# Kernel tuning notes

Measured on AMD Instinct MI355X. Metric: run time of the kernel, lower is better.

The kernel has to match this reference:

```python
import jax, jax.numpy as jnp
import numpy as np

NEG_SLOPE = 0.01  # torch F.leaky_relu default


def _graph_conv(x, W, b, src, dst, n_dst):
    """DGL GraphConv, norm='both': out = D_dst^{-1/2} A^T (D_src^{-1/2} x W) + b.
    Degrees clamped to min 1 (DGL behavior). src/dst are edge endpoint indices.
    """
    n_src = x.shape[0]
    ones = jnp.ones(src.shape[0], dtype=x.dtype)
    out_deg = jnp.zeros(n_src, dtype=x.dtype).at[src].add(ones)
    in_deg = jnp.zeros(n_dst, dtype=x.dtype).at[dst].add(ones)
    inv_s = jax.lax.rsqrt(jnp.maximum(out_deg, 1.0))
    inv_d = jax.lax.rsqrt(jnp.maximum(in_deg, 1.0))
    # weight first (in_feats >= out_feats path in DGL; math identical either way)
    feat = (x * inv_s[:, None]) @ W                      # [n_src, out]
    agg = jax.ops.segment_sum(feat[src], dst, num_segments=n_dst)  # SpMM
    return agg * inv_d[:, None] + b


def setup_inputs() -> dict:
    key = jax.random.key(0)
    ks = jax.random.split(key, 16)
    Nc, Ng, F, H, O = 50000, 30000, 128, 128, 128
    Ecc, Ecg, Egc = 500000, 400000, 400000
    inp = {
        "x_chem": jax.random.normal(ks[0], (Nc, F), jnp.float32),
        "x_gene": jax.random.normal(ks[1], (Ng, F), jnp.float32),
        "src_cc": jax.random.randint(ks[2], (Ecc,), 0, Nc, jnp.int32),
        "dst_cc": jax.random.randint(ks[3], (Ecc,), 0, Nc, jnp.int32),
        "src_cg": jax.random.randint(ks[4], (Ecg,), 0, Nc, jnp.int32),
        "dst_cg": jax.random.randint(ks[5], (Ecg,), 0, Ng, jnp.int32),
        "src_gc": jax.random.randint(ks[6], (Egc,), 0, Ng, jnp.int32),
        "dst_gc": jax.random.randint(ks[7], (Egc,), 0, Nc, jnp.int32),
    }
    scale1 = 1.0 / np.sqrt(F)
    scale2 = 1.0 / np.sqrt(H)
    inp["W1_cc"] = jax.random.normal(ks[8], (F, H), jnp.float32) * scale1
    inp["W1_cg"] = jax.random.normal(ks[9], (F, H), jnp.float32) * scale1
    inp["W1_gc"] = jax.random.normal(ks[10], (F, H), jnp.float32) * scale1
    inp["W2_cc"] = jax.random.normal(ks[11], (H, O), jnp.float32) * scale2
    inp["W2_cg"] = jax.random.normal(ks[12], (H, O), jnp.float32) * scale2
    inp["W2_gc"] = jax.random.normal(ks[13], (H, O), jnp.float32) * scale2
    for name, d in [("b1_cc", H), ("b1_cg", H), ("b1_gc", H), ("b2_cc", O), ("b2_cg", O), ("b2_gc", O)]:
        inp[name] = jnp.zeros((d,), jnp.float32)
    return inp


def reference(x_chem, x_gene, src_cc, dst_cc, src_cg, dst_cg, src_gc, dst_gc,
              W1_cc, b1_cc, W1_cg, b1_cg, W1_gc, b1_gc,
              W2_cc, b2_cc, W2_cg, b2_cg, W2_gc, b2_gc):
    Nc, Ng = x_chem.shape[0], x_gene.shape[0]
    # --- layer 1: HeteroGraphConv with sum aggregation across relations ---
    h1_chem = (_graph_conv(x_chem, W1_cc, b1_cc, src_cc, dst_cc, Nc)
               + _graph_conv(x_gene, W1_gc, b1_gc, src_gc, dst_gc, Nc))
    h1_gene = _graph_conv(x_chem, W1_cg, b1_cg, src_cg, dst_cg, Ng)
    h1_chem = jax.nn.leaky_relu(h1_chem, NEG_SLOPE)
    h1_gene = jax.nn.leaky_relu(h1_gene, NEG_SLOPE)
    # --- layer 2 ---
    h2_chem = (_graph_conv(h1_chem, W2_cc, b2_cc, src_cc, dst_cc, Nc)
               + _graph_conv(h1_gene, W2_gc, b2_gc, src_gc, dst_gc, Nc))
    return h2_chem
```

## Files before the change

kernel.cpp:

```cpp
#include <hip/hip_runtime.h>
#include <math.h>

#define NEG_SLOPE 0.01f
#define ELLW 40

typedef float f4 __attribute__((ext_vector_type(4)));
typedef __bf16 bf16x8 __attribute__((ext_vector_type(8)));
typedef __bf16 bf16x4 __attribute__((ext_vector_type(4)));
typedef _Float16 h4 __attribute__((ext_vector_type(4)));
typedef _Float16 h8 __attribute__((ext_vector_type(8)));

__global__ __launch_bounds__(256) void prep_w_zero(
    const float* __restrict__ W0, const float* __restrict__ W1,
    const float* __restrict__ W2, const float* __restrict__ W3,
    const float* __restrict__ W4, __bf16* __restrict__ H, __bf16* __restrict__ L,
    int* __restrict__ zp, int zN)
{
    const int b = blockIdx.x;
    if (b < 320) {
        const int y = b >> 6;
        const float* W = y == 0 ? W0 : y == 1 ? W1 : y == 2 ? W2 : y == 3 ? W3 : W4;
        int idx = (b & 63) * 256 + threadIdx.x;
        int k = idx >> 7, n = idx & 127;
        float w = W[idx];
        __bf16 h = (__bf16)w;
        __bf16 l = (__bf16)(w - (float)h);
        H[(size_t)y * 16384 + n * 128 + k] = h;
        L[(size_t)y * 16384 + n * 128 + k] = l;
    } else {
        int i = (b - 320) * 256 + threadIdx.x;
        if (i < zN) zp[i] = 0;
    }
}

template <int RELU, typename T>
__device__ __forceinline__ void gemm_core(const T* __restrict__ A,
    const __bf16* __restrict__ Bh, const __bf16* __restrict__ Bl,
    _Float16* __restrict__ C, int M, int row0, int tid,
    __bf16 (*Ah)[136], __bf16 (*Al)[136])
{
    if constexpr (sizeof(T) == 4) {
#pragma unroll
        for (int it = 0; it < 8; ++it) {
            int idx4 = it * 256 + tid;
            int r = idx4 >> 5;
            int c = (idx4 & 31) << 2;
            int rg = row0 + r;
            f4 v = {0.f, 0.f, 0.f, 0.f};
            if (rg < M) v = *(const f4*)(A + (size_t)rg * 128 + c);
            if (RELU) {
#pragma unroll
                for (int j = 0; j < 4; ++j) v[j] = v[j] >= 0.f ? v[j] : v[j] * NEG_SLOPE;
            }
            bf16x4 hv, lv;
#pragma unroll
            for (int j = 0; j < 4; ++j) {
                __bf16 h = (__bf16)v[j];
                hv[j] = h;
                lv[j] = (__bf16)(v[j] - (float)h);
            }
            *(bf16x4*)&Ah[r][c] = hv;
            *(bf16x4*)&Al[r][c] = lv;
        }
    } else {
#pragma unroll
        for (int it = 0; it < 4; ++it) {
            int idx8 = it * 256 + tid;
            int r = idx8 >> 4;
            int c = (idx8 & 15) << 3;
            int rg = row0 + r;
            h8 v8 = {};
            if (rg < M) v8 = *(const h8*)(A + (size_t)rg * 128 + c);
            bf16x8 hv, lv;
#pragma unroll
            for (int j = 0; j < 8; ++j) {
                float v = (float)v8[j];
                if (RELU) v = v >= 0.f ? v : v * NEG_SLOPE;
                __bf16 h = (__bf16)v;
                hv[j] = h;
                lv[j] = (__bf16)(v - (float)h);
            }
            *(bf16x8*)&Ah[r][c] = hv;
            *(bf16x8*)&Al[r][c] = lv;
        }
    }
    __syncthreads();

    const int lane = tid & 63;
    const int wid = tid >> 6;
    const int lm = lane & 15;
    const int lq = lane >> 4;
    const int mbase = (wid & 1) * 32;
    const int nbase = (wid >> 1) * 64;

    f4 acc[2][4] = {};
#pragma unroll
    for (int kc = 0; kc < 4; ++kc) {
        const int koff = kc * 32 + lq * 8;
        bf16x8 ah[2], al[2], bh[4], bl[4];
#pragma unroll
        for (int mi = 0; mi < 2; ++mi) {
            ah[mi] = *(const bf16x8*)&Ah[mbase + mi * 16 + lm][koff];
            al[mi] = *(const bf16x8*)&Al[mbase + mi * 16 + lm][koff];
        }
#pragma unroll
        for (int ni = 0; ni < 4; ++ni) {
            size_t boff = (size_t)(nbase + ni * 16 + lm) * 128 + koff;
            bh[ni] = *(const bf16x8*)(Bh + boff);
            bl[ni] = *(const bf16x8*)(Bl + boff);
        }
#pragma unroll
        for (int mi = 0; mi < 2; ++mi)
#pragma unroll
            for (int ni = 0; ni < 4; ++ni) {
                acc[mi][ni] = __builtin_amdgcn_mfma_f32_16x16x32_bf16(ah[mi], bh[ni], acc[mi][ni], 0, 0, 0);
                acc[mi][ni] = __builtin_amdgcn_mfma_f32_16x16x32_bf16(al[mi], bh[ni], acc[mi][ni], 0, 0, 0);
                acc[mi][ni] = __builtin_amdgcn_mfma_f32_16x16x32_bf16(ah[mi], bl[ni], acc[mi][ni], 0, 0, 0);
            }
    }

#pragma unroll
    for (int mi = 0; mi < 2; ++mi) {
        int rbase = row0 + mbase + mi * 16 + lq * 4;
#pragma unroll
        for (int r = 0; r < 4; ++r) {
            int row = rbase + r;
            if (row < M) {
#pragma unroll
                for (int ni = 0; ni < 4; ++ni)
                    C[(size_t)row * 128 + nbase + ni * 16 + lm] = (_Float16)acc[mi][ni][r];
            }
        }
    }
}

__global__ __launch_bounds__(256) void fused_build_gemm(
    const int* __restrict__ s0, const int* __restrict__ d0, int* sd0, int* c0, unsigned short* e0, int E0, int B0,
    const int* __restrict__ s1, const int* __restrict__ d1, int* sd1, int* c1, unsigned short* e1, int E1, int B1,
    const int* __restrict__ s2, const int* __restrict__ d2, int* sd2, int* c2, unsigned short* e2, int E2,
    const float* __restrict__ xc, const float* __restrict__ xg,
    const __bf16* __restrict__ wt_h, const __bf16* __restrict__ wt_l,
    _Float16* __restrict__ t_cg, _Float16* __restrict__ t_cc, _Float16* __restrict__ t_gc,
    int Nc, int Ng, int gBc, int G, int EB)
{
    __shared__ __bf16 Ah[64][136];
    __shared__ __bf16 Al[64][136];
    const int idx = blockIdx.x;
    const int r7 = idx % 7, q = idx / 7;
    if (r7 < 2) {
        int g = q * 2 + r7;
        if (g >= G) return;
        if (g < gBc)
            gemm_core<0>(xc, wt_h, wt_l, t_cg, Nc, g * 64, threadIdx.x, Ah, Al);
        else if (g < 2 * gBc)
            gemm_core<0>(xc, wt_h + 16384, wt_l + 16384, t_cc, Nc, (g - gBc) * 64, threadIdx.x, Ah, Al);
        else
            gemm_core<0>(xg, wt_h + 2 * 16384, wt_l + 2 * 16384, t_gc, Ng, (g - 2 * gBc) * 64, threadIdx.x, Ah, Al);
    } else {
        int eb = q * 5 + (r7 - 2);
        if (eb >= EB) return;
        const int* src; const int* dst; int* sdeg; int* cnt; unsigned short* ell; int E; int base;
        if (eb < B0)            { src = s0; dst = d0; sdeg = sd0; cnt = c0; ell = e0; E = E0; base = eb; }
        else if (eb < B0 + B1)  { src = s1; dst = d1; sdeg = sd1; cnt = c1; ell = e1; E = E1; base = eb - B0; }
        else                    { src = s2; dst = d2; sdeg = sd2; cnt = c2; ell = e2; E = E2; base = eb - B0 - B1; }
        int i0 = base * 512 + threadIdx.x;
        int i1 = i0 + 256;
        int sa = -1, da = 0, sb = -1, db = 0;
        if (i0 < E) { sa = src[i0]; da = dst[i0]; }
        if (i1 < E) { sb = src[i1]; db = dst[i1]; }
        if (sa >= 0) atomicAdd(&sdeg[sa], 1);
        if (sb >= 0) atomicAdd(&sdeg[sb], 1);
        if (sa >= 0) {
            int p = atomicAdd(&cnt[da], 1);
            if (p < ELLW) ell[da * ELLW + p] = (unsigned short)sa;
        }
        if (sb >= 0) {
            int p = atomicAdd(&cnt[db], 1);
            if (p < ELLW) ell[db * ELLW + p] = (unsigned short)sb;
        }
    }
}

__global__ __launch_bounds__(256) void gemm2_both(
    const _Float16* __restrict__ h1c, const _Float16* __restrict__ h1g,
    const __bf16* __restrict__ wt_h, const __bf16* __restrict__ wt_l,
    _Float16* __restrict__ t_cc, _Float16* __restrict__ t_gc, int Nc, int Ng, int gBc)
{
    __shared__ __bf16 Ah[64][136];
    __shared__ __bf16 Al[64][136];
    if ((int)blockIdx.x < gBc)
        gemm_core<1>(h1c, wt_h + 3 * 16384, wt_l + 3 * 16384, t_cc, Nc, blockIdx.x * 64, threadIdx.x, Ah, Al);
    else
        gemm_core<1>(h1g, wt_h + 4 * 16384, wt_l + 4 * 16384, t_gc, Ng, (blockIdx.x - gBc) * 64, threadIdx.x, Ah, Al);
}

__device__ __forceinline__ void rel_accum8(const _Float16* __restrict__ feat,
    const unsigned short* __restrict__ cp, int n, const int* __restrict__ sdeg,
    int grp, int c8, float* acc)
{
    int i = grp;
    for (; i + 4 < n; i += 8) {
        int q0 = cp[i], q1 = cp[i + 4];
        float w0 = rsqrtf(fmaxf((float)sdeg[q0], 1.0f));
        float w1 = rsqrtf(fmaxf((float)sdeg[q1], 1.0f));
        h8 v0 = *(const h8*)(feat + (size_t)q0 * 128 + c8);
        h8 v1 = *(const h8*)(feat + (size_t)q1 * 128 + c8);
#pragma unroll
        for (int j = 0; j < 8; ++j) acc[j] += (float)v0[j] * w0;
#pragma unroll
        for (int j = 0; j < 8; ++j) acc[j] += (float)v1[j] * w1;
    }
    if (i < n) {
        int q0 = cp[i];
        float w0 = rsqrtf(fmaxf((float)sdeg[q0], 1.0f));
        h8 v0 = *(const h8*)(feat + (size_t)q0 * 128 + c8);
#pragma unroll
        for (int j = 0; j < 8; ++j) acc[j] += (float)v0[j] * w0;
    }
}

__device__ __forceinline__ void xgrp_sum8(float* a)
{
#pragma unroll
    for (int j = 0; j < 8; ++j) {
        a[j] += __shfl_xor(a[j], 16);
        a[j] += __shfl_xor(a[j], 32);
    }
}

__global__ __launch_bounds__(256) void gather_l1(
    const _Float16* __restrict__ t_cg, const unsigned short* __restrict__ ell_cg,
    const int* __restrict__ cnt_cg, const int* __restrict__ degs_cg,
    const _Float16* __restrict__ f_cc, const unsigned short* __restrict__ ell_cc,
    const int* __restrict__ cnt_cc, const int* __restrict__ degs_cc,
    const _Float16* __restrict__ t_gc, const unsigned short* __restrict__ ell_gc,
    const int* __restrict__ cnt_gc, const int* __restrict__ degs_gc,
    const float* __restrict__ b1_cg, const float* __restrict__ b1_cc, const float* __restrict__ b1_gc,
    _Float16* __restrict__ h1_gene, _Float16* __restrict__ h1_chem, int Ng, int Nc, int Bg)
{
    const int lane = threadIdx.x & 63;
    const int grp = lane >> 4;
    const int c8 = (lane & 15) << 3;
    if ((int)blockIdx.x < Bg) {
        int row = blockIdx.x * 4 + (threadIdx.x >> 6);
        if (row >= Ng) return;
        int n = cnt_cg[row];
        float wd = rsqrtf(fmaxf((float)n, 1.0f));
        if (n > ELLW) n = ELLW;
        float acc[8] = {};
        rel_accum8(t_cg, ell_cg + row * ELLW, n, degs_cg, grp, c8, acc);
#pragma unroll
        for (int j = 0; j < 8; ++j) acc[j] *= wd;
        xgrp_sum8(acc);
        if (grp == 0) {
            f4 blo = *(const f4*)(b1_cg + c8);
            f4 bhi = *(const f4*)(b1_cg + c8 + 4);
            h8 o;
#pragma unroll
            for (int j = 0; j < 4; ++j) o[j] = (_Float16)(acc[j] + blo[j]);
#pragma unroll
            for (int j = 0; j < 4; ++j) o[4 + j] = (_Float16)(acc[4 + j] + bhi[j]);
            *(h8*)(h1_gene + (size_t)row * 128 + c8) = o;
        }
    } else {
        int row = (blockIdx.x - Bg) * 4 + (threadIdx.x >> 6);
        if (row >= Nc) return;
        int na = cnt_cc[row];
        float wa = rsqrtf(fmaxf((float)na, 1.0f));
        if (na > ELLW) na = ELLW;
        float accA[8] = {};
        rel_accum8(f_cc, ell_cc + row * ELLW, na, degs_cc, grp, c8, accA);
        int nb = cnt_gc[row];
        float wb = rsqrtf(fmaxf((float)nb, 1.0f));
        if (nb > ELLW) nb = ELLW;
        float accB[8] = {};
        rel_accum8(t_gc, ell_gc + row * ELLW, nb, degs_gc, grp, c8, accB);
        float r[8];
#pragma unroll
        for (int j = 0; j < 8; ++j) r[j] = accA[j] * wa + accB[j] * wb;
        xgrp_sum8(r);
        if (grp == 0) {
            f4 b0lo = *(const f4*)(b1_cc + c8);
            f4 b0hi = *(const f4*)(b1_cc + c8 + 4);
            f4 b1lo = *(const f4*)(b1_gc + c8);
            f4 b1hi = *(const f4*)(b1_gc + c8 + 4);
            h8 o;
#pragma unroll
            for (int j = 0; j < 4; ++j) o[j] = (_Float16)(r[j] + b0lo[j] + b1lo[j]);
#pragma unroll
            for (int j = 0; j < 4; ++j) o[4 + j] = (_Float16)(r[4 + j] + b0hi[j] + b1hi[j]);
            *(h8*)(h1_chem + (size_t)row * 128 + c8) = o;
        }
    }
}

__global__ __launch_bounds__(256) void gather_l2(
    const _Float16* __restrict__ fA, const unsigned short* __restrict__ ellA,
    const int* __restrict__ cntA, const int* __restrict__ degsA,
    const _Float16* __restrict__ fB, const unsigned short* __restrict__ ellB,
    const int* __restrict__ cntB, const int* __restrict__ degsB,
    const float* __restrict__ bA, const float* __restrict__ bB,
    float* __restrict__ out, int Nd)
{
    const int lane = threadIdx.x & 63;
    const int grp = lane >> 4;
    const int c8 = (lane & 15) << 3;
    int row = blockIdx.x * 4 + (threadIdx.x >> 6);
    if (row >= Nd) return;
    int na = cntA[row];
    float wa = rsqrtf(fmaxf((float)na, 1.0f));
    if (na > ELLW) na = ELLW;
    float accA[8] = {};
    rel_accum8(fA, ellA + row * ELLW, na, degsA, grp, c8, accA);
    int nb = cntB[row];
    float wb = rsqrtf(fmaxf((float)nb, 1.0f));
    if (nb > ELLW) nb = ELLW;
    float accB[8] = {};
    rel_accum8(fB, ellB + row * ELLW, nb, degsB, grp, c8, accB);
    float r[8];
#pragma unroll
    for (int j = 0; j < 8; ++j) r[j] = accA[j] * wa + accB[j] * wb;
    xgrp_sum8(r);
    if (grp == 0) {
        f4 balo = *(const f4*)(bA + c8);
        f4 bahi = *(const f4*)(bA + c8 + 4);
        f4 bblo = *(const f4*)(bB + c8);
        f4 bbhi = *(const f4*)(bB + c8 + 4);
        f4 olo, ohi;
#pragma unroll
        for (int j = 0; j < 4; ++j) olo[j] = r[j] + balo[j] + bblo[j];
#pragma unroll
        for (int j = 0; j < 4; ++j) ohi[j] = r[4 + j] + bahi[j] + bbhi[j];
        *(f4*)(out + (size_t)row * 128 + c8) = olo;
        *(f4*)(out + (size_t)row * 128 + c8 + 4) = ohi;
    }
}

extern "C" void kernel_launch(void* const* d_in, const int* in_sizes, int n_in,
                              void* d_out, int out_size, void* d_ws, size_t ws_size,
                              hipStream_t stream)
{
    const float* x_chem = (const float*)d_in[0];
    const float* x_gene = (const float*)d_in[1];
    const int* src_cc = (const int*)d_in[2];
    const int* dst_cc = (const int*)d_in[3];
    const int* src_cg = (const int*)d_in[4];
    const int* dst_cg = (const int*)d_in[5];
    const int* src_gc = (const int*)d_in[6];
    const int* dst_gc = (const int*)d_in[7];
    const float* W1_cc = (const float*)d_in[8];
    const float* W1_cg = (const float*)d_in[9];
    const float* W1_gc = (const float*)d_in[10];
    const float* W2_cc = (const float*)d_in[11];
    const float* W2_gc = (const float*)d_in[13];
    const float* b1_cc = (const float*)d_in[14];
    const float* b1_cg = (const float*)d_in[15];
    const float* b1_gc = (const float*)d_in[16];
    const float* b2_cc = (const float*)d_in[17];
    const float* b2_gc = (const float*)d_in[19];
    (void)n_in; (void)out_size; (void)ws_size;

    const int Nc = in_sizes[0] / 128;
    const int Ng = in_sizes[1] / 128;
    const int Ecc = in_sizes[2];
    const int Ecg = in_sizes[4];
    const int Egc = in_sizes[6];

    int* cnt_cc  = (int*)d_ws;
    int* cnt_cg  = cnt_cc + Nc;
    int* cnt_gc  = cnt_cg + Ng;
    int* degs_cc = cnt_gc + Nc;
    int* degs_cg = degs_cc + Nc;
    int* degs_gc = degs_cg + Nc;
    const int degTotal = 4 * Nc + 2 * Ng;
    unsigned short* ell_cc = (unsigned short*)(degs_gc + Ng);
    unsigned short* ell_cg = ell_cc + (size_t)Nc * ELLW;
    unsigned short* ell_gc = ell_cg + (size_t)Ng * ELLW;
    size_t off = (size_t)((char*)(ell_gc + (size_t)Nc * ELLW) - (char*)d_ws);
    off = (off + 255) & ~(size_t)255;
    _Float16* h1_chem = (_Float16*)((char*)d_ws + off);
    _Float16* h1_gene = h1_chem + (size_t)Nc * 128;
    _Float16* tmp_cg  = h1_gene + (size_t)Ng * 128;
    _Float16* tmp_gc  = tmp_cg + (size_t)Nc * 128;
    _Float16* tmp_cc  = tmp_gc + (size_t)Ng * 128;
    __bf16* wt_h = (__bf16*)(tmp_cc + (size_t)Nc * 128);
    __bf16* wt_l = wt_h + 5 * 16384;
    float* outF = (float*)d_out;

    dim3 blk(256);
    const int B0 = (Ecc + 511) / 512, B1 = (Ecg + 511) / 512, B2 = (Egc + 511) / 512;
    const int EB = B0 + B1 + B2;
    const int gBc = (Nc + 63) / 64, gBg = (Ng + 63) / 64;
    const int G = 2 * gBc + gBg;
    int Q = (G + 1) / 2;
    if ((EB + 4) / 5 > Q) Q = (EB + 4) / 5;
    const int T = 7 * Q;

    const int zB = (degTotal + 255) / 256;
    prep_w_zero<<<320 + zB, blk, 0, stream>>>(W1_cg, W1_cc, W1_gc, W2_cc, W2_gc,
        wt_h, wt_l, (int*)d_ws, degTotal);

    fused_build_gemm<<<T, blk, 0, stream>>>(
        src_cc, dst_cc, degs_cc, cnt_cc, ell_cc, Ecc, B0,
        src_cg, dst_cg, degs_cg, cnt_cg, ell_cg, Ecg, B1,
        src_gc, dst_gc, degs_gc, cnt_gc, ell_gc, Egc,
        x_chem, x_gene, wt_h, wt_l, tmp_cg, tmp_cc, tmp_gc,
        Nc, Ng, gBc, G, EB);

    const int Bg = (Ng + 3) / 4, Bc = (Nc + 3) / 4;
    gather_l1<<<Bg + Bc, blk, 0, stream>>>(
        tmp_cg, ell_cg, cnt_cg, degs_cg,
        tmp_cc, ell_cc, cnt_cc, degs_cc,
        tmp_gc, ell_gc, cnt_gc, degs_gc,
        b1_cg, b1_cc, b1_gc, h1_gene, h1_chem, Ng, Nc, Bg);

    gemm2_both<<<gBc + gBg, blk, 0, stream>>>(h1_chem, h1_gene, wt_h, wt_l,
        tmp_cg, tmp_gc, Nc, Ng, gBc);

    gather_l2<<<Bc, blk, 0, stream>>>(
        tmp_cg, ell_cc, cnt_cc, degs_cc,
        tmp_gc, ell_gc, cnt_gc, degs_gc,
        b2_cc, b2_gc, outF, Nc);
}
```

Measured before the change: 373.9 us.

## Pre-scale feature tables by source-degree norm instead of per-edge rsqrt in gathers

Moves the D_src^{-1/2} normalisation out of the per-edge gather loops. Layer-1 tables are rescaled in a new scale_tables pass, and layer-2 tables get the factor in the GEMM epilogue. The gathers then drop the per-edge random sdeg loads and rsqrt, at the cost of an extra read-modify-write pass over the layer-1 tables and one extra launch. The edge-build blocks also drop from 512 to 256 edges per block, which doubles their count.

```diff
diff --git a/kernel.cpp b/kernel.cpp
--- a/kernel.cpp
+++ b/kernel.cpp
@@ -33,10 +33,10 @@
     }
 }
 
-template <int RELU, typename T>
+template <int RELU, int SCALE, typename T>
 __device__ __forceinline__ void gemm_core(const T* __restrict__ A,
     const __bf16* __restrict__ Bh, const __bf16* __restrict__ Bl,
-    _Float16* __restrict__ C, int M, int row0, int tid,
+    _Float16* __restrict__ C, const int* __restrict__ rdeg, int M, int row0, int tid,
     __bf16 (*Ah)[136], __bf16 (*Al)[136])
 {
     if constexpr (sizeof(T) == 4) {
@@ -126,9 +126,11 @@
         for (int r = 0; r < 4; ++r) {
             int row = rbase + r;
             if (row < M) {
+                float s = 1.0f;
+                if (SCALE) s = rsqrtf(fmaxf((float)rdeg[row], 1.0f));
 #pragma unroll
                 for (int ni = 0; ni < 4; ++ni)
-                    C[(size_t)row * 128 + nbase + ni * 16 + lm] = (_Float16)acc[mi][ni][r];
+                    C[(size_t)row * 128 + nbase + ni * 16 + lm] = (_Float16)(acc[mi][ni][r] * s);
             }
         }
     }
@@ -151,11 +153,11 @@
         int g = q * 2 + r7;
         if (g >= G) return;
         if (g < gBc)
-            gemm_core<0>(xc, wt_h, wt_l, t_cg, Nc, g * 64, threadIdx.x, Ah, Al);
+            gemm_core<0, 0>(xc, wt_h, wt_l, t_cg, (const int*)nullptr, Nc, g * 64, threadIdx.x, Ah, Al);
         else if (g < 2 * gBc)
-            gemm_core<0>(xc, wt_h + 16384, wt_l + 16384, t_cc, Nc, (g - gBc) * 64, threadIdx.x, Ah, Al);
+            gemm_core<0, 0>(xc, wt_h + 16384, wt_l + 16384, t_cc, (const int*)nullptr, Nc, (g - gBc) * 64, threadIdx.x, Ah, Al);
         else
-            gemm_core<0>(xg, wt_h + 2 * 16384, wt_l + 2 * 16384, t_gc, Ng, (g - 2 * gBc) * 64, threadIdx.x, Ah, Al);
+            gemm_core<0, 0>(xg, wt_h + 2 * 16384, wt_l + 2 * 16384, t_gc, (const int*)nullptr, Ng, (g - 2 * gBc) * 64, threadIdx.x, Ah, Al);
     } else {
         int eb = q * 5 + (r7 - 2);
         if (eb >= EB) return;
@@ -163,59 +165,73 @@
         if (eb < B0)            { src = s0; dst = d0; sdeg = sd0; cnt = c0; ell = e0; E = E0; base = eb; }
         else if (eb < B0 + B1)  { src = s1; dst = d1; sdeg = sd1; cnt = c1; ell = e1; E = E1; base = eb - B0; }
         else                    { src = s2; dst = d2; sdeg = sd2; cnt = c2; ell = e2; E = E2; base = eb - B0 - B1; }
-        int i0 = base * 512 + threadIdx.x;
-        int i1 = i0 + 256;
-        int sa = -1, da = 0, sb = -1, db = 0;
-        if (i0 < E) { sa = src[i0]; da = dst[i0]; }
-        if (i1 < E) { sb = src[i1]; db = dst[i1]; }
-        if (sa >= 0) atomicAdd(&sdeg[sa], 1);
-        if (sb >= 0) atomicAdd(&sdeg[sb], 1);
-        if (sa >= 0) {
-            int p = atomicAdd(&cnt[da], 1);
-            if (p < ELLW) ell[da * ELLW + p] = (unsigned short)sa;
-        }
-        if (sb >= 0) {
-            int p = atomicAdd(&cnt[db], 1);
-            if (p < ELLW) ell[db * ELLW + p] = (unsigned short)sb;
-        }
-    }
+        int i = base * 256 + threadIdx.x;
+        if (i < E) {
+            int s = src[i];
+            int d = dst[i];
+            atomicAdd(&sdeg[s], 1);
+            int p = atomicAdd(&cnt[d], 1);
+            if (p < ELLW) ell[d * ELLW + p] = (unsigned short)s;
+        }
+    }
+}
+
+__global__ __launch_bounds__(256) void scale_tables(
+    _Float16* __restrict__ t_cg, const int* __restrict__ degs_cg,
+    _Float16* __restrict__ t_cc, const int* __restrict__ degs_cc,
+    _Float16* __restrict__ t_gc, const int* __restrict__ degs_gc,
+    int Nc, int Ng)
+{
+    int idx = blockIdx.x * 256 + threadIdx.x;
+    int gr = idx >> 4;
+    int c8 = (idx & 15) << 3;
+    int total = 2 * Nc + Ng;
+    if (gr >= total) return;
+    _Float16* p;
+    int deg;
+    if (gr < Nc)            { p = t_cg + (size_t)gr * 128 + c8;            deg = degs_cg[gr]; }
+    else if (gr < 2 * Nc)   { p = t_cc + (size_t)(gr - Nc) * 128 + c8;     deg = degs_cc[gr - Nc]; }
+    else                    { p = t_gc + (size_t)(gr - 2 * Nc) * 128 + c8; deg = degs_gc[gr - 2 * Nc]; }
+    float s = rsqrtf(fmaxf((float)deg, 1.0f));
+    h8 v = *(const h8*)p;
+#pragma unroll
+    for (int j = 0; j < 8; ++j) v[j] = (_Float16)((float)v[j] * s);
+    *(h8*)p = v;
 }
 
 __global__ __launch_bounds__(256) void gemm2_both(
     const _Float16* __restrict__ h1c, const _Float16* __restrict__ h1g,
     const __bf16* __restrict__ wt_h, const __bf16* __restrict__ wt_l,
+    const int* __restrict__ degs_cc, const int* __restrict__ degs_gc,
     _Float16* __restrict__ t_cc, _Float16* __restrict__ t_gc, int Nc, int Ng, int gBc)
 {
     __shared__ __bf16 Ah[64][136];
     __shared__ __bf16 Al[64][136];
     if ((int)blockIdx.x < gBc)
-        gemm_core<1>(h1c, wt_h + 3 * 16384, wt_l + 3 * 16384, t_cc, Nc, blockIdx.x * 64, threadIdx.x, Ah, Al);
+        gemm_core<1, 1>(h1c, wt_h + 3 * 16384, wt_l + 3 * 16384, t_cc, degs_cc, Nc, blockIdx.x * 64, threadIdx.x, Ah, Al);
     else
-        gemm_core<1>(h1g, wt_h + 4 * 16384, wt_l + 4 * 16384, t_gc, Ng, (blockIdx.x - gBc) * 64, threadIdx.x, Ah, Al);
+        gemm_core<1, 1>(h1g, wt_h + 4 * 16384, wt_l + 4 * 16384, t_gc, degs_gc, Ng, (blockIdx.x - gBc) * 64, threadIdx.x, Ah, Al);
 }
 
 __device__ __forceinline__ void rel_accum8(const _Float16* __restrict__ feat,
-    const unsigned short* __restrict__ cp, int n, const int* __restrict__ sdeg,
+    const unsigned short* __restrict__ cp, int n,
     int grp, int c8, float* acc)
 {
     int i = grp;
     for (; i + 4 < n; i += 8) {
         int q0 = cp[i], q1 = cp[i + 4];
-        float w0 = rsqrtf(fmaxf((float)sdeg[q0], 1.0f));
-        float w1 = rsqrtf(fmaxf((float)sdeg[q1], 1.0f));
         h8 v0 = *(const h8*)(feat + (size_t)q0 * 128 + c8);
         h8 v1 = *(const h8*)(feat + (size_t)q1 * 128 + c8);
 #pragma unroll
-        for (int j = 0; j < 8; ++j) acc[j] += (float)v0[j] * w0;
-#pragma unroll
-        for (int j = 0; j < 8; ++j) acc[j] += (float)v1[j] * w1;
+        for (int j = 0; j < 8; ++j) acc[j] += (float)v0[j];
+#pragma unroll
+        for (int j = 0; j < 8; ++j) acc[j] += (float)v1[j];
     }
     if (i < n) {
         int q0 = cp[i];
-        float w0 = rsqrtf(fmaxf((float)sdeg[q0], 1.0f));
         h8 v0 = *(const h8*)(feat + (size_t)q0 * 128 + c8);
 #pragma unroll
-        for (int j = 0; j < 8; ++j) acc[j] += (float)v0[j] * w0;
+        for (int j = 0; j < 8; ++j) acc[j] += (float)v0[j];
     }
 }
 
@@ -230,11 +246,11 @@
 
 __global__ __launch_bounds__(256) void gather_l1(
     const _Float16* __restrict__ t_cg, const unsigned short* __restrict__ ell_cg,
-    const int* __restrict__ cnt_cg, const int* __restrict__ degs_cg,
+    const int* __restrict__ cnt_cg,
     const _Float16* __restrict__ f_cc, const unsigned short* __restrict__ ell_cc,
-    const int* __restrict__ cnt_cc, const int* __restrict__ degs_cc,
+    const int* __restrict__ cnt_cc,
     const _Float16* __restrict__ t_gc, const unsigned short* __restrict__ ell_gc,
-    const int* __restrict__ cnt_gc, const int* __restrict__ degs_gc,
+    const int* __restrict__ cnt_gc,
     const float* __restrict__ b1_cg, const float* __restrict__ b1_cc, const float* __restrict__ b1_gc,
     _Float16* __restrict__ h1_gene, _Float16* __restrict__ h1_chem, int Ng, int Nc, int Bg)
 {
@@ -248,7 +264,7 @@
         float wd = rsqrtf(fmaxf((float)n, 1.0f));
         if (n > ELLW) n = ELLW;
         float acc[8] = {};
-        rel_accum8(t_cg, ell_cg + row * ELLW, n, degs_cg, grp, c8, acc);
+        rel_accum8(t_cg, ell_cg + row * ELLW, n, grp, c8, acc);
 #pragma unroll
         for (int j = 0; j < 8; ++j) acc[j] *= wd;
         xgrp_sum8(acc);
@@ -269,12 +285,12 @@
         float wa = rsqrtf(fmaxf((float)na, 1.0f));
         if (na > ELLW) na = ELLW;
         float accA[8] = {};
-        rel_accum8(f_cc, ell_cc + row * ELLW, na, degs_cc, grp, c8, accA);
+        rel_accum8(f_cc, ell_cc + row * ELLW, na, grp, c8, accA);
         int nb = cnt_gc[row];
         float wb = rsqrtf(fmaxf((float)nb, 1.0f));
         if (nb > ELLW) nb = ELLW;
         float accB[8] = {};
-        rel_accum8(t_gc, ell_gc + row * ELLW, nb, degs_gc, grp, c8, accB);
+        rel_accum8(t_gc, ell_gc + row * ELLW, nb, grp, c8, accB);
         float r[8];
 #pragma unroll
         for (int j = 0; j < 8; ++j) r[j] = accA[j] * wa + accB[j] * wb;
@@ -296,9 +312,9 @@
 
 __global__ __launch_bounds__(256) void gather_l2(
     const _Float16* __restrict__ fA, const unsigned short* __restrict__ ellA,
-    const int* __restrict__ cntA, const int* __restrict__ degsA,
+    const int* __restrict__ cntA,
     const _Float16* __restrict__ fB, const unsigned short* __restrict__ ellB,
-    const int* __restrict__ cntB, const int* __restrict__ degsB,
+    const int* __restrict__ cntB,
     const float* __restrict__ bA, const float* __restrict__ bB,
     float* __restrict__ out, int Nd)
 {
@@ -311,12 +327,12 @@
     float wa = rsqrtf(fmaxf((float)na, 1.0f));
     if (na > ELLW) na = ELLW;
     float accA[8] = {};
-    rel_accum8(fA, ellA + row * ELLW, na, degsA, grp, c8, accA);
+    rel_accum8(fA, ellA + row * ELLW, na, grp, c8, accA);
     int nb = cntB[row];
     float wb = rsqrtf(fmaxf((float)nb, 1.0f));
     if (nb > ELLW) nb = ELLW;
     float accB[8] = {};
-    rel_accum8(fB, ellB + row * ELLW, nb, degsB, grp, c8, accB);
+    rel_accum8(fB, ellB + row * ELLW, nb, grp, c8, accB);
     float r[8];
 #pragma unroll
     for (int j = 0; j < 8; ++j) r[j] = accA[j] * wa + accB[j] * wb;
@@ -388,7 +404,7 @@
     float* outF = (float*)d_out;
 
     dim3 blk(256);
-    const int B0 = (Ecc + 511) / 512, B1 = (Ecg + 511) / 512, B2 = (Egc + 511) / 512;
+    const int B0 = (Ecc + 255) / 256, B1 = (Ecg + 255) / 256, B2 = (Egc + 255) / 256;
     const int EB = B0 + B1 + B2;
     const int gBc = (Nc + 63) / 64, gBg = (Ng + 63) / 64;
     const int G = 2 * gBc + gBg;
@@ -407,18 +423,22 @@
         x_chem, x_gene, wt_h, wt_l, tmp_cg, tmp_cc, tmp_gc,
         Nc, Ng, gBc, G, EB);
 
+    const int rowsTotal = 2 * Nc + Ng;
+    const int sB = (rowsTotal * 16 + 255) / 256;
+    scale_tables<<<sB, blk, 0, stream>>>(tmp_cg, degs_cg, tmp_cc, degs_cc, tmp_gc, degs_gc, Nc, Ng);
+
     const int Bg = (Ng + 3) / 4, Bc = (Nc + 3) / 4;
     gather_l1<<<Bg + Bc, blk, 0, stream>>>(
-        tmp_cg, ell_cg, cnt_cg, degs_cg,
-        tmp_cc, ell_cc, cnt_cc, degs_cc,
-        tmp_gc, ell_gc, cnt_gc, degs_gc,
+        tmp_cg, ell_cg, cnt_cg,
+        tmp_cc, ell_cc, cnt_cc,
+        tmp_gc, ell_gc, cnt_gc,
         b1_cg, b1_cc, b1_gc, h1_gene, h1_chem, Ng, Nc, Bg);
 
     gemm2_both<<<gBc + gBg, blk, 0, stream>>>(h1_chem, h1_gene, wt_h, wt_l,
-        tmp_cg, tmp_gc, Nc, Ng, gBc);
+        degs_cc, degs_gc, tmp_cg, tmp_gc, Nc, Ng, gBc);
 
     gather_l2<<<Bc, blk, 0, stream>>>(
-        tmp_cg, ell_cc, cnt_cc, degs_cc,
-        tmp_gc, ell_gc, cnt_gc, degs_gc,
+        tmp_cg, ell_cc, cnt_cc,
+        tmp_gc, ell_gc, cnt_gc,
         b2_cc, b2_gc, outF, Nc);
 }
```

After: 376.7 us. About the same (+0.7%).
